# Performance work log

Measured on AMD Instinct MI355X. Metric: run time of the kernel, lower is better.

## Reference

```python
import math
import jax, jax.numpy as jnp
import numpy as np

B, C, F_, W = 4, 2, 512, 1024
NH = 8
HD = F_ // NH            # 64 head dim
ROT = HD // 2            # 32 rotated dims
NFREQ = ROT // 2         # 16 base freqs ('pixel': linspace(1, max_freq/2, dim//2)*pi)


def mc_linear(x, w_pw):
    # x: [b,c,f_in,w], w_pw: [c, f_out, f_in] -> [b,c,f_out,w]
    return jnp.einsum('bchw,cgh->bcgw', x, w_pw)


def apply_rope(t, freqs):
    # t: [b,c,n,w,d]; freqs: [w, rot_dim] (already pair-repeated)
    rot_dim = freqs.shape[-1]
    t_rot, t_pass = t[..., :rot_dim], t[..., rot_dim:]
    cos, sin = jnp.cos(freqs), jnp.sin(freqs)
    x1, x2 = t_rot[..., 0::2], t_rot[..., 1::2]
    rh = jnp.stack([-x2, x1], axis=-1).reshape(t_rot.shape)  # rotate_half (interleaved pairs)
    return jnp.concatenate([t_rot * cos + rh * sin, t_pass], axis=-1)


def setup_inputs() -> dict:
    key = jax.random.key(0)
    ks = jax.random.split(key, 6)
    x = jax.random.normal(ks[0], (B, C, F_, W), dtype=jnp.float32)
    bound = 1.0 / math.sqrt(F_)
    def w(k):
        return jax.random.uniform(k, (C, F_, F_), minval=-bound, maxval=bound, dtype=jnp.float32)
    wq, wk, wv, wo = w(ks[1]), w(ks[2]), w(ks[3]), w(ks[4])
    # learned 'pixel' freqs: linspace(1., max_freq/2=5., NFREQ) * pi
    freqs_param = (jnp.linspace(1.0, 5.0, NFREQ) * math.pi).astype(jnp.float32)
    return {"x": x, "wq": wq, "wk": wk, "wv": wv, "wo": wo, "freqs_param": freqs_param}


def reference(x, wq, wk, wv, wo, freqs_param):
    b, c, h, w = x.shape
    def heads(t):  # [b,c,h,w] -> [b,c,NH,w,HD]
        return t.transpose(0, 1, 3, 2).reshape(b, c, w, NH, HD).transpose(0, 1, 3, 2, 4)
    pos = jnp.arange(w, dtype=jnp.float32)
    freqs = jnp.repeat(pos[:, None] * freqs_param[None, :], 2, axis=-1)  # [w, ROT]
    # NOTE: original module uses q_proj for q, k, and v (k_proj/v_proj unused)
    q = apply_rope(heads(mc_linear(x, wq)), freqs)
    k = apply_rope(heads(mc_linear(x, wq)), freqs)
    v = heads(mc_linear(x, wq))
    qk = jnp.einsum('bcnqd,bcnkd->bcnqk', q, k) / math.sqrt(h)
    a = jnp.einsum('bcnqk,bcnkd->bcnqd', jax.nn.softmax(qk, axis=-1), v)
    a = a.transpose(0, 1, 3, 2, 4).reshape(b, c, w, NH * HD).transpose(0, 1, 3, 2)  # [b,c,h,w]
    return mc_linear(a, wo)
```

## Files before the change

### kernel.cpp

```cpp
#include <hip/hip_runtime.h>
#include <hip/hip_bf16.h>
#include <math.h>

#define B_ 4
#define C_ 2
#define F_ 512
#define W_ 1024
#define NH_ 8
#define HD_ 64
#define ROT_ 32
#define NFREQ_ 16
#define BC_ (B_*C_)

#define QSC_ 0.2525048f

typedef short bf16x8 __attribute__((ext_vector_type(8)));
typedef float f32x4  __attribute__((ext_vector_type(4)));
typedef float f32x16 __attribute__((ext_vector_type(16)));
typedef unsigned short u16;
typedef unsigned int   u32;

#if __has_builtin(__builtin_amdgcn_exp2f)
#define EXP2(x) __builtin_amdgcn_exp2f(x)
#else
#define EXP2(x) exp2f(x)
#endif

__device__ __forceinline__ u16 f2bf(float f) {
    union { float f; u32 u; } v; v.f = f;
    u32 r = (v.u + 0x7fffu + ((v.u >> 16) & 1u)) >> 16;
    return (u16)r;
}
__device__ __forceinline__ float bf2f(u16 h) {
    union { u32 u; float f; } v; v.u = ((u32)h) << 16;
    return v.f;
}
__device__ __forceinline__ f32x4 mfma16(bf16x8 a, bf16x8 b, f32x4 c) {
    return __builtin_amdgcn_mfma_f32_16x16x32_bf16(a, b, c, 0, 0, 0);
}
__device__ __forceinline__ f32x16 mfma32(bf16x8 a, bf16x8 b, f32x16 c) {
    return __builtin_amdgcn_mfma_f32_32x32x16_bf16(a, b, c, 0, 0, 0);
}
__device__ __forceinline__ void gload16(const u16* g, u16* l) {
    __builtin_amdgcn_global_load_lds(
        (const __attribute__((address_space(1))) u32*)g,
        (__attribute__((address_space(3))) u32*)l, 16, 0, 0);
}
__device__ __forceinline__ u32 pk2(float lo, float hi) {
    __hip_bfloat162 h = __float22bfloat162_rn(make_float2(lo, hi));
    union { __hip_bfloat162 b; u32 u; } cv; cv.b = h; return cv.u;
}
__device__ __forceinline__ void pl32swap(u32& a, u32& b) {
    asm volatile("v_permlane32_swap_b32 %0, %1" : "+v"(a), "+v"(b));
}


__global__ __launch_bounds__(256)
void conv_hi(const float* __restrict__ src, u16* __restrict__ hi, int n) {
    int i = (blockIdx.x * 256 + threadIdx.x) * 4;
    if (i >= n) return;
    float4 v = *(const float4*)(src + i);
    ushort4 h;
    h.x = f2bf(v.x); h.y = f2bf(v.y); h.z = f2bf(v.z); h.w = f2bf(v.w);
    *(ushort4*)(hi + i) = h;
}

__global__ __launch_bounds__(256)
void conv_split(const float* __restrict__ src, u16* __restrict__ hi, u16* __restrict__ lo, int n) {
    int i = (blockIdx.x * 256 + threadIdx.x) * 4;
    if (i >= n) return;
    float4 v = *(const float4*)(src + i);
    ushort4 h, l;
    h.x = f2bf(v.x); l.x = f2bf(v.x - bf2f(h.x));
    h.y = f2bf(v.y); l.y = f2bf(v.y - bf2f(h.y));
    h.z = f2bf(v.z); l.z = f2bf(v.z - bf2f(h.z));
    h.w = f2bf(v.w); l.w = f2bf(v.w - bf2f(h.w));
    *(ushort4*)(hi + i) = h;
    *(ushort4*)(lo + i) = l;
}

__global__ __launch_bounds__(256)
void conv_xt(const float* __restrict__ x, u16* __restrict__ xh) {
    __shared__ float T[64][65];
    const int t = threadIdx.x;
    const int h0 = blockIdx.x * 64, w0 = blockIdx.y * 64, bc = blockIdx.z;
    {
        const int hl = t >> 2, wc = (t & 3) * 16;
        const float* src = x + ((size_t)bc * F_ + h0 + hl) * W_ + w0 + wc;
        #pragma unroll
        for (int z = 0; z < 4; ++z)
            *(float4*)(&T[hl][wc + z * 4]) = *(const float4*)(src + z * 4);
    }
    __syncthreads();
    {
        const int wl = t >> 2, hc = (t & 3) * 16;
        u16 hv[16];
        #pragma unroll
        for (int z = 0; z < 16; ++z) hv[z] = f2bf(T[hc + z][wl]);
        size_t base = ((size_t)bc * W_ + w0 + wl) * F_ + h0 + hc;
        *(uint4*)(xh + base)     = *(uint4*)(hv);
        *(uint4*)(xh + base + 8) = *(uint4*)(hv + 8);
    }
}

__global__ __launch_bounds__(256)
void trig_fill(const float* __restrict__ fp, float2* __restrict__ tbl) {
    int idx = blockIdx.x * 256 + threadIdx.x;
    if (idx >= W_ * NFREQ_) return;
    int w = idx >> 4, j = idx & 15;
    float th = (float)w * fp[j];
    float s, c;
    sincosf(th, &s, &c);
    tbl[idx] = make_float2(c, s);
}

template<int MODE>
__global__ __launch_bounds__(256)
void gemm2(const u16* __restrict__ Ah_, const u16* __restrict__ Al_,
           const u16* __restrict__ Bh_, const u16* __restrict__ Bl_,
           u16* __restrict__ Vout, u16* __restrict__ Qout,
           float* __restrict__ Fout, const float2* __restrict__ trig)
{
    __shared__ u16 sh[16384];
    u16* Ash = sh;
    u16* Bsh = sh + 4096;
    u16* Asl = sh + 8192;
    u16* Bsl = sh + 12288;

    const int tid = threadIdx.x, lane = tid & 63, wid = tid >> 6;
    const int m0 = blockIdx.x * 128, n0 = blockIdx.y * 128, bc = blockIdx.z, c = bc % C_;
    const u16* Abh = Ah_ + (size_t)c * F_ * F_;
    const u16* Abl = MODE ? Al_ + (size_t)c * F_ * F_ : (const u16*)nullptr;
    const u16* Bbh = Bh_ + (size_t)bc * W_ * F_;
    const u16* Bbl = MODE ? Bl_ + (size_t)bc * W_ * F_ : (const u16*)nullptr;

    f32x4 acc[4][4] = {};
    const int mb = (wid >> 1) * 64, nb = (wid & 1) * 64;
    const int r_in = lane >> 2, tsl = lane & 3;

    for (int k0 = 0; k0 < F_; k0 += 32) {
        #pragma unroll
        for (int h = 0; h < 2; ++h) {
            const int row = h * 64 + wid * 16 + r_in;
            const int ts  = tsl ^ (row & 3);
            const int lb  = (h * 64 + wid * 16) * 32;
            gload16(Abh + (size_t)(m0 + row) * F_ + k0 + ts * 8, Ash + lb);
            gload16(Bbh + (size_t)(n0 + row) * F_ + k0 + ts * 8, Bsh + lb);
            if (MODE) {
                gload16(Abl + (size_t)(m0 + row) * F_ + k0 + ts * 8, Asl + lb);
                gload16(Bbl + (size_t)(n0 + row) * F_ + k0 + ts * 8, Bsl + lb);
            }
        }
        __syncthreads();

        bf16x8 fah[4], fal[4];
        #pragma unroll
        for (int i = 0; i < 4; ++i) {
            const int row = mb + i * 16 + (lane & 15);
            const int idx = row * 32 + (((lane >> 4) ^ (row & 3)) << 3);
            fah[i] = *(const bf16x8*)(&Ash[idx]);
            if (MODE) fal[i] = *(const bf16x8*)(&Asl[idx]);
        }
        #pragma unroll
        for (int j = 0; j < 4; ++j) {
            const int rowb = nb + j * 16 + (lane & 15);
            const int idxb = rowb * 32 + (((lane >> 4) ^ (rowb & 3)) << 3);
            bf16x8 bh = *(const bf16x8*)(&Bsh[idxb]);
            #pragma unroll
            for (int i = 0; i < 4; ++i)
                acc[i][j] = mfma16(fah[i], bh, acc[i][j]);
            if (MODE) {
                bf16x8 bl = *(const bf16x8*)(&Bsl[idxb]);
                #pragma unroll
                for (int i = 0; i < 4; ++i) {
                    acc[i][j] = mfma16(fah[i], bl, acc[i][j]);
                    acc[i][j] = mfma16(fal[i], bh, acc[i][j]);
                }
            }
        }
        __syncthreads();
    }

    #pragma unroll
    for (int i = 0; i < 4; ++i) {
        const int gr = m0 + mb + i * 16 + (lane >> 4) * 4;
        #pragma unroll
        for (int j = 0; j < 4; ++j) {
            const int wc = n0 + nb + j * 16 + (lane & 15);
            #pragma unroll
            for (int r = 0; r < 4; ++r) {
                const size_t ad = ((size_t)bc * F_ + gr + r) * W_ + wc;
                if (MODE == 1) Fout[ad] = acc[i][j][r];
                else           Vout[ad] = f2bf(acc[i][j][r]);
            }
        }
    }

    if (MODE == 0) {
        __syncthreads();
        u16* Qt = sh + wid * 4096;
        #pragma unroll
        for (int j = 0; j < 4; ++j) {
            const int wl = j * 16 + (lane & 15);
            const int wg = n0 + nb + wl;
            #pragma unroll
            for (int i = 0; i < 4; ++i) {
                const int ddb = i * 16 + (lane >> 4) * 4;
                float q[4];
                if (i < 2) {
                    #pragma unroll
                    for (int p = 0; p < 2; ++p) {
                        const int fidx = (ddb >> 1) + p;
                        float2 cs = trig[wg * NFREQ_ + fidx];
                        float e = acc[i][j][2 * p], o = acc[i][j][2 * p + 1];
                        q[2 * p]     = (e * cs.x - o * cs.y) * QSC_;
                        q[2 * p + 1] = (o * cs.x + e * cs.y) * QSC_;
                    }
                } else {
                    #pragma unroll
                    for (int r = 0; r < 4; ++r) q[r] = acc[i][j][r] * QSC_;
                }
                #pragma unroll
                for (int r = 0; r < 4; ++r)
                    Qt[wl * 64 + ((ddb + r) ^ ((wl & 7) << 3))] = f2bf(q[r]);
            }
        }
        const int wl = lane;
        const int wg = n0 + nb + wl;
        const int head = (m0 + mb) >> 6;
        const size_t qbase = (((size_t)bc * NH_ + head) * W_ + wg) * 64;
        #pragma unroll
        for (int s = 0; s < 8; ++s) {
            uint4 v = *(const uint4*)(&Qt[wl * 64 + ((s ^ (wl & 7)) << 3)]);
            *(uint4*)(&Qout[qbase + s * 8]) = v;
        }
    }
}

__global__ __launch_bounds__(256)
void attn2(const u16* __restrict__ Qt, const u16* __restrict__ Vg,
           u16* __restrict__ Ah, u16* __restrict__ Al)
{
    __shared__ u16 Ks[4096];
    __shared__ u16 Vs[4096];
    const int tid = threadIdx.x, lane = tid & 63, wid = tid >> 6;
    const int q0 = blockIdx.x * 128, head = blockIdx.y, bc = blockIdx.z;
    const u16* qb = Qt + ((size_t)bc * NH_ + head) * W_ * 64;
    const u16* vb = Vg + ((size_t)bc * F_ + head * HD_) * W_;

    const int qcol = lane & 31, hi = lane >> 5;

    bf16x8 qf[4];
    {
        const u16* qrow = qb + (size_t)(q0 + wid * 32 + qcol) * 64 + hi * 8;
        #pragma unroll
        for (int ks = 0; ks < 4; ++ks)
            qf[ks] = *(const bf16x8*)(qrow + ks * 16);
    }

    f32x16 o0, o1;
    #pragma unroll
    for (int i = 0; i < 16; ++i) { o0[i] = 0.f; o1[i] = 0.f; }
    float lsum = 0.f;

    const int srow = lane >> 3, st = lane & 7;

    for (int kt = 0; kt < 16; ++kt) {
        const int k0 = kt * 64;
        #pragma unroll
        for (int p = 0; p < 2; ++p) {
            const int rb = wid * 16 + p * 8;
            const int r  = rb + srow;
            const int ts = st ^ (r & 7);
            gload16(qb + (size_t)(k0 + r) * 64 + ts * 8, Ks + rb * 64);
            gload16(vb + (size_t)r * W_ + k0 + ts * 8,   Vs + rb * 64);
        }
        __syncthreads();

        f32x16 s0, s1;
        #pragma unroll
        for (int i = 0; i < 16; ++i) { s0[i] = 0.f; s1[i] = 0.f; }
        #pragma unroll
        for (int ks = 0; ks < 4; ++ks) {
            const int sl = ks * 2 + hi;
            const int kA = qcol;
            const int kB = 32 + qcol;
            bf16x8 kf0 = *(const bf16x8*)(Ks + kA * 64 + ((sl ^ (kA & 7)) << 3));
            bf16x8 kf1 = *(const bf16x8*)(Ks + kB * 64 + ((sl ^ (kB & 7)) << 3));
            s0 = mfma32(kf0, qf[ks], s0);
            s1 = mfma32(kf1, qf[ks], s1);
        }

        float p0[16], p1[16];
        #pragma unroll
        for (int i = 0; i < 16; ++i) { p0[i] = EXP2(s0[i]); p1[i] = EXP2(s1[i]); }
        float part = 0.f;
        #pragma unroll
        for (int i = 0; i < 16; ++i) part += p0[i] + p1[i];
        lsum += part;

        bf16x8 pf[4];
        #pragma unroll
        for (int kb = 0; kb < 2; ++kb) {
            const float* pp = kb ? p1 : p0;
            #pragma unroll
            for (int f = 0; f < 2; ++f) {
                u32 a1 = pk2(pp[f*8+0], pp[f*8+1]);
                u32 a2 = pk2(pp[f*8+2], pp[f*8+3]);
                u32 b1 = pk2(pp[f*8+4], pp[f*8+5]);
                u32 b2 = pk2(pp[f*8+6], pp[f*8+7]);
                pl32swap(a1, b1);
                pl32swap(a2, b2);
                union { u32 w[4]; bf16x8 v; } u;
                u.w[0] = a1; u.w[1] = a2; u.w[2] = b1; u.w[3] = b2;
                pf[kb * 2 + f] = u.v;
            }
        }

        #pragma unroll
        for (int ks2 = 0; ks2 < 4; ++ks2) {
            const int sl = ks2 * 2 + hi;
            const int d0r = qcol;
            const int d1r = 32 + qcol;
            bf16x8 vf0 = *(const bf16x8*)(Vs + d0r * 64 + ((sl ^ (d0r & 7)) << 3));
            bf16x8 vf1 = *(const bf16x8*)(Vs + d1r * 64 + ((sl ^ (d1r & 7)) << 3));
            o0 = mfma32(vf0, pf[ks2], o0);
            o1 = mfma32(vf1, pf[ks2], o1);
        }
        __syncthreads();
    }

    lsum += __shfl_xor(lsum, 32);
    const float inv = 1.f / lsum;

    const int wrow = q0 + wid * 32 + qcol;
    const size_t rowbase = ((size_t)bc * W_ + wrow) * F_ + head * HD_;
    #pragma unroll
    for (int dblk = 0; dblk < 2; ++dblk) {
        const f32x16 ov = dblk ? o1 : o0;
        const int coloff = dblk * 32;
        #pragma unroll
        for (int pr = 0; pr < 8; ++pr) {
            const float v1 = ov[2 * pr]     * inv;
            const float v2 = ov[2 * pr + 1] * inv;
            const int drow = ((2 * pr) & 3) + 8 * (pr >> 1) + 4 * hi;
            const u16 h1 = f2bf(v1), h2 = f2bf(v2);
            const u16 l1 = f2bf(v1 - bf2f(h1)), l2 = f2bf(v2 - bf2f(h2));
            *(u32*)(Ah + rowbase + coloff + drow) = (u32)h1 | ((u32)h2 << 16);
            *(u32*)(Al + rowbase + coloff + drow) = (u32)l1 | ((u32)l2 << 16);
        }
    }
}

extern "C" void kernel_launch(void* const* d_in, const int* in_sizes, int n_in,
                              void* d_out, int out_size, void* d_ws, size_t ws_size,
                              hipStream_t stream) {
    const float* x  = (const float*)d_in[0];
    const float* wq = (const float*)d_in[1];
    const float* wo = (const float*)d_in[4];
    const float* fp = (const float*)d_in[5];
    float* out = (float*)d_out;

    char* w8 = (char*)d_ws;
    const size_t MB = 1024 * 1024;
    u16* xh   = (u16*)(w8);
    u16* wqh  = (u16*)(w8 + 8 * MB);
    u16* woh  = (u16*)(w8 + 9 * MB);
    u16* wol  = (u16*)(w8 + 10 * MB);
    float2* trig = (float2*)(w8 + 11 * MB);
    u16* qbuf = (u16*)(w8 + 12 * MB);
    u16* vbuf = (u16*)(w8 + 20 * MB);
    u16* al   = (u16*)(w8 + 28 * MB);
    u16* ah   = xh;

    const int nw = C_ * F_ * F_;
    conv_hi<<<nw / 1024, 256, 0, stream>>>(wq, wqh, nw);
    conv_split<<<nw / 1024, 256, 0, stream>>>(wo, woh, wol, nw);
    trig_fill<<<(W_ * NFREQ_) / 256, 256, 0, stream>>>(fp, trig);
    conv_xt<<<dim3(F_ / 64, W_ / 64, BC_), 256, 0, stream>>>(x, xh);

    gemm2<0><<<dim3(F_ / 128, W_ / 128, BC_), 256, 0, stream>>>(
        wqh, nullptr, xh, nullptr, vbuf, qbuf, nullptr, trig);

    attn2<<<dim3(W_ / 128, NH_, BC_), 256, 0, stream>>>(qbuf, vbuf, ah, al);

    gemm2<1><<<dim3(F_ / 128, W_ / 128, BC_), 256, 0, stream>>>(
        woh, wol, ah, al, nullptr, nullptr, out, nullptr);
}
```

Measured before the change: 163.8 us.

## Double-buffer LDS loads in GEMM and attention kernels, merge prep kernels

Both GEMM kernels and the attention kernel now use two shared-memory buffers, so the async global-to-LDS loads for the next k-tile are issued before computing on the current one. This overlaps memory latency with MFMA work, at the cost of doubled LDS use, which may lower occupancy. The GEMM LDS swizzle changes from row&3 to (row>>1)&3 to reduce bank conflicts. The three weight/trig preparation kernels are merged into one launch to cut launch overhead.

```diff
diff --git a/kernel.cpp b/kernel.cpp
--- a/kernel.cpp
+++ b/kernel.cpp
@@ -26,6 +26,8 @@
 #define EXP2(x) exp2f(x)
 #endif
 
+#define VDRAIN() asm volatile("s_waitcnt vmcnt(0)" ::: "memory")
+
 __device__ __forceinline__ u16 f2bf(float f) {
     union { float f; u32 u; } v; v.f = f;
     u32 r = (v.u + 0x7fffu + ((v.u >> 16) & 1u)) >> 16;
@@ -54,29 +56,37 @@
     asm volatile("v_permlane32_swap_b32 %0, %1" : "+v"(a), "+v"(b));
 }
 
-
 __global__ __launch_bounds__(256)
-void conv_hi(const float* __restrict__ src, u16* __restrict__ hi, int n) {
-    int i = (blockIdx.x * 256 + threadIdx.x) * 4;
-    if (i >= n) return;
-    float4 v = *(const float4*)(src + i);
-    ushort4 h;
-    h.x = f2bf(v.x); h.y = f2bf(v.y); h.z = f2bf(v.z); h.w = f2bf(v.w);
-    *(ushort4*)(hi + i) = h;
-}
-
-__global__ __launch_bounds__(256)
-void conv_split(const float* __restrict__ src, u16* __restrict__ hi, u16* __restrict__ lo, int n) {
-    int i = (blockIdx.x * 256 + threadIdx.x) * 4;
-    if (i >= n) return;
-    float4 v = *(const float4*)(src + i);
-    ushort4 h, l;
-    h.x = f2bf(v.x); l.x = f2bf(v.x - bf2f(h.x));
-    h.y = f2bf(v.y); l.y = f2bf(v.y - bf2f(h.y));
-    h.z = f2bf(v.z); l.z = f2bf(v.z - bf2f(h.z));
-    h.w = f2bf(v.w); l.w = f2bf(v.w - bf2f(h.w));
-    *(ushort4*)(hi + i) = h;
-    *(ushort4*)(lo + i) = l;
+void prep(const float* __restrict__ wq, const float* __restrict__ wo,
+          const float* __restrict__ fp,
+          u16* __restrict__ wqh, u16* __restrict__ woh, u16* __restrict__ wol,
+          float2* __restrict__ trig)
+{
+    const int b = blockIdx.x, t = threadIdx.x;
+    if (b < 512) {
+        int i = (b * 256 + t) * 4;
+        float4 v = *(const float4*)(wq + i);
+        ushort4 h;
+        h.x = f2bf(v.x); h.y = f2bf(v.y); h.z = f2bf(v.z); h.w = f2bf(v.w);
+        *(ushort4*)(wqh + i) = h;
+    } else if (b < 1024) {
+        int i = ((b - 512) * 256 + t) * 4;
+        float4 v = *(const float4*)(wo + i);
+        ushort4 h, l;
+        h.x = f2bf(v.x); l.x = f2bf(v.x - bf2f(h.x));
+        h.y = f2bf(v.y); l.y = f2bf(v.y - bf2f(h.y));
+        h.z = f2bf(v.z); l.z = f2bf(v.z - bf2f(h.z));
+        h.w = f2bf(v.w); l.w = f2bf(v.w - bf2f(h.w));
+        *(ushort4*)(woh + i) = h;
+        *(ushort4*)(wol + i) = l;
+    } else {
+        int idx = (b - 1024) * 256 + t;
+        int w = idx >> 4, j = idx & 15;
+        float th = (float)w * fp[j];
+        float s, c;
+        sincosf(th, &s, &c);
+        trig[idx] = make_float2(c, s);
+    }
 }
 
 __global__ __launch_bounds__(256)
@@ -103,73 +113,71 @@
     }
 }
 
-__global__ __launch_bounds__(256)
-void trig_fill(const float* __restrict__ fp, float2* __restrict__ tbl) {
-    int idx = blockIdx.x * 256 + threadIdx.x;
-    if (idx >= W_ * NFREQ_) return;
-    int w = idx >> 4, j = idx & 15;
-    float th = (float)w * fp[j];
-    float s, c;
-    sincosf(th, &s, &c);
-    tbl[idx] = make_float2(c, s);
-}
-
 template<int MODE>
 __global__ __launch_bounds__(256)
-void gemm2(const u16* __restrict__ Ah_, const u16* __restrict__ Al_,
+void gemm3(const u16* __restrict__ Ah_, const u16* __restrict__ Al_,
            const u16* __restrict__ Bh_, const u16* __restrict__ Bl_,
            u16* __restrict__ Vout, u16* __restrict__ Qout,
            float* __restrict__ Fout, const float2* __restrict__ trig)
 {
-    __shared__ u16 sh[16384];
-    u16* Ash = sh;
-    u16* Bsh = sh + 4096;
-    u16* Asl = sh + 8192;
-    u16* Bsl = sh + 12288;
+    constexpr int BUFS = MODE ? 16384 : 8192;
+    __shared__ u16 sh[2 * BUFS];
 
     const int tid = threadIdx.x, lane = tid & 63, wid = tid >> 6;
     const int m0 = blockIdx.x * 128, n0 = blockIdx.y * 128, bc = blockIdx.z, c = bc % C_;
     const u16* Abh = Ah_ + (size_t)c * F_ * F_;
-    const u16* Abl = MODE ? Al_ + (size_t)c * F_ * F_ : (const u16*)nullptr;
+    const u16* Abl = MODE ? (Al_ + (size_t)c * F_ * F_) : (const u16*)nullptr;
     const u16* Bbh = Bh_ + (size_t)bc * W_ * F_;
-    const u16* Bbl = MODE ? Bl_ + (size_t)bc * W_ * F_ : (const u16*)nullptr;
+    const u16* Bbl = MODE ? (Bl_ + (size_t)bc * W_ * F_) : (const u16*)nullptr;
 
     f32x4 acc[4][4] = {};
     const int mb = (wid >> 1) * 64, nb = (wid & 1) * 64;
     const int r_in = lane >> 2, tsl = lane & 3;
 
-    for (int k0 = 0; k0 < F_; k0 += 32) {
+    auto STAGE = [&](int k0, int buf) {
+        u16* base = sh + buf * BUFS;
         #pragma unroll
         for (int h = 0; h < 2; ++h) {
             const int row = h * 64 + wid * 16 + r_in;
-            const int ts  = tsl ^ (row & 3);
+            const int ts  = tsl ^ ((row >> 1) & 3);
             const int lb  = (h * 64 + wid * 16) * 32;
-            gload16(Abh + (size_t)(m0 + row) * F_ + k0 + ts * 8, Ash + lb);
-            gload16(Bbh + (size_t)(n0 + row) * F_ + k0 + ts * 8, Bsh + lb);
-            if (MODE) {
-                gload16(Abl + (size_t)(m0 + row) * F_ + k0 + ts * 8, Asl + lb);
-                gload16(Bbl + (size_t)(n0 + row) * F_ + k0 + ts * 8, Bsl + lb);
+            gload16(Abh + (size_t)(m0 + row) * F_ + k0 + ts * 8, base + lb);
+            gload16(Bbh + (size_t)(n0 + row) * F_ + k0 + ts * 8, base + 4096 + lb);
+            if constexpr (MODE) {
+                gload16(Abl + (size_t)(m0 + row) * F_ + k0 + ts * 8, base + 8192 + lb);
+                gload16(Bbl + (size_t)(n0 + row) * F_ + k0 + ts * 8, base + 12288 + lb);
             }
         }
-        __syncthreads();
+    };
+
+    STAGE(0, 0);
+    VDRAIN();
+    __syncthreads();
+    int cur = 0;
+    for (int kt = 0; kt < 16; ++kt) {
+        if (kt < 15) STAGE((kt + 1) * 32, cur ^ 1);
+        const u16* Ash = sh + cur * BUFS;
+        const u16* Bsh = Ash + 4096;
+        const u16* Asl = MODE ? Ash + 8192  : Ash;
+        const u16* Bsl = MODE ? Ash + 12288 : Ash;
 
         bf16x8 fah[4], fal[4];
         #pragma unroll
         for (int i = 0; i < 4; ++i) {
             const int row = mb + i * 16 + (lane & 15);
-            const int idx = row * 32 + (((lane >> 4) ^ (row & 3)) << 3);
+            const int idx = row * 32 + (((lane >> 4) ^ ((row >> 1) & 3)) << 3);
             fah[i] = *(const bf16x8*)(&Ash[idx]);
-            if (MODE) fal[i] = *(const bf16x8*)(&Asl[idx]);
+            if constexpr (MODE) fal[i] = *(const bf16x8*)(&Asl[idx]);
         }
         #pragma unroll
         for (int j = 0; j < 4; ++j) {
             const int rowb = nb + j * 16 + (lane & 15);
-            const int idxb = rowb * 32 + (((lane >> 4) ^ (rowb & 3)) << 3);
+            const int idxb = rowb * 32 + (((lane >> 4) ^ ((rowb >> 1) & 3)) << 3);
             bf16x8 bh = *(const bf16x8*)(&Bsh[idxb]);
             #pragma unroll
             for (int i = 0; i < 4; ++i)
                 acc[i][j] = mfma16(fah[i], bh, acc[i][j]);
-            if (MODE) {
+            if constexpr (MODE) {
                 bf16x8 bl = *(const bf16x8*)(&Bsl[idxb]);
                 #pragma unroll
                 for (int i = 0; i < 4; ++i) {
@@ -178,7 +186,9 @@
                 }
             }
         }
+        VDRAIN();
         __syncthreads();
+        cur ^= 1;
     }
 
     #pragma unroll
@@ -190,13 +200,13 @@
             #pragma unroll
             for (int r = 0; r < 4; ++r) {
                 const size_t ad = ((size_t)bc * F_ + gr + r) * W_ + wc;
-                if (MODE == 1) Fout[ad] = acc[i][j][r];
-                else           Vout[ad] = f2bf(acc[i][j][r]);
+                if constexpr (MODE == 1) Fout[ad] = acc[i][j][r];
+                else                     Vout[ad] = f2bf(acc[i][j][r]);
             }
         }
     }
 
-    if (MODE == 0) {
+    if constexpr (MODE == 0) {
         __syncthreads();
         u16* Qt = sh + wid * 4096;
         #pragma unroll
@@ -238,17 +248,17 @@
 }
 
 __global__ __launch_bounds__(256)
-void attn2(const u16* __restrict__ Qt, const u16* __restrict__ Vg,
+void attn3(const u16* __restrict__ Qt, const u16* __restrict__ Vg,
            u16* __restrict__ Ah, u16* __restrict__ Al)
 {
-    __shared__ u16 Ks[4096];
-    __shared__ u16 Vs[4096];
+    __shared__ u16 sh[16384];
     const int tid = threadIdx.x, lane = tid & 63, wid = tid >> 6;
     const int q0 = blockIdx.x * 128, head = blockIdx.y, bc = blockIdx.z;
     const u16* qb = Qt + ((size_t)bc * NH_ + head) * W_ * 64;
     const u16* vb = Vg + ((size_t)bc * F_ + head * HD_) * W_;
 
     const int qcol = lane & 31, hi = lane >> 5;
+    const int srow = lane >> 3, st = lane & 7;
 
     bf16x8 qf[4];
     {
@@ -263,19 +273,28 @@
     for (int i = 0; i < 16; ++i) { o0[i] = 0.f; o1[i] = 0.f; }
     float lsum = 0.f;
 
-    const int srow = lane >> 3, st = lane & 7;
-
-    for (int kt = 0; kt < 16; ++kt) {
+    auto STAGE = [&](int kt, int buf) {
         const int k0 = kt * 64;
+        u16* Ksb = sh + buf * 8192;
+        u16* Vsb = Ksb + 4096;
         #pragma unroll
         for (int p = 0; p < 2; ++p) {
             const int rb = wid * 16 + p * 8;
             const int r  = rb + srow;
             const int ts = st ^ (r & 7);
-            gload16(qb + (size_t)(k0 + r) * 64 + ts * 8, Ks + rb * 64);
-            gload16(vb + (size_t)r * W_ + k0 + ts * 8,   Vs + rb * 64);
-        }
-        __syncthreads();
+            gload16(qb + (size_t)(k0 + r) * 64 + ts * 8, Ksb + rb * 64);
+            gload16(vb + (size_t)r * W_ + k0 + ts * 8,   Vsb + rb * 64);
+        }
+    };
+
+    STAGE(0, 0);
+    VDRAIN();
+    __syncthreads();
+    int cur = 0;
+    for (int kt = 0; kt < 16; ++kt) {
+        if (kt < 15) STAGE(kt + 1, cur ^ 1);
+        const u16* Ks = sh + cur * 8192;
+        const u16* Vs = Ks + 4096;
 
         f32x16 s0, s1;
         #pragma unroll
@@ -327,7 +346,9 @@
             o0 = mfma32(vf0, pf[ks2], o0);
             o1 = mfma32(vf1, pf[ks2], o1);
         }
+        VDRAIN();
         __syncthreads();
+        cur ^= 1;
     }
 
     lsum += __shfl_xor(lsum, 32);
@@ -373,17 +394,14 @@
     u16* al   = (u16*)(w8 + 28 * MB);
     u16* ah   = xh;
 
-    const int nw = C_ * F_ * F_;
-    conv_hi<<<nw / 1024, 256, 0, stream>>>(wq, wqh, nw);
-    conv_split<<<nw / 1024, 256, 0, stream>>>(wo, woh, wol, nw);
-    trig_fill<<<(W_ * NFREQ_) / 256, 256, 0, stream>>>(fp, trig);
+    prep<<<1088, 256, 0, stream>>>(wq, wo, fp, wqh, woh, wol, trig);
     conv_xt<<<dim3(F_ / 64, W_ / 64, BC_), 256, 0, stream>>>(x, xh);
 
-    gemm2<0><<<dim3(F_ / 128, W_ / 128, BC_), 256, 0, stream>>>(
+    gemm3<0><<<dim3(F_ / 128, W_ / 128, BC_), 256, 0, stream>>>(
         wqh, nullptr, xh, nullptr, vbuf, qbuf, nullptr, trig);
 
-    attn2<<<dim3(W_ / 128, NH_, BC_), 256, 0, stream>>>(qbuf, vbuf, ah, al);
-
-    gemm2<1><<<dim3(F_ / 128, W_ / 128, BC_), 256, 0, stream>>>(
+    attn3<<<dim3(W_ / 128, NH_, BC_), 256, 0, stream>>>(qbuf, vbuf, ah, al);
+
+    gemm3<1><<<dim3(F_ / 128, W_ / 128, BC_), 256, 0, stream>>>(
         woh, wol, ah, al, nullptr, nullptr, out, nullptr);
 }
```

Measured after the change: 148.6 us. 9.3% less time.
